# Kernel tuning notes

Measured on AMD Instinct MI355X. Metric: run time of the kernel, lower is better.

Reference implementation:

```python
import jax, jax.numpy as jnp
import numpy as np

ALPHA = 3.0


def _conv3x3(x, W, b):
    # x: [N, C, H, W]; W: [O, I, 3, 3]; SAME padding, stride 1 (matches Conv2d(dim, dim, 3, 1, 1))
    y = jax.lax.conv_general_dilated(
        x, W, window_strides=(1, 1), padding='SAME',
        dimension_numbers=('NCHW', 'OIHW', 'NCHW'))
    return y + b[None, :, None, None]


def setup_inputs() -> dict:
    key = jax.random.key(0)
    k = jax.random.split(key, 5)
    b, m, z, x, y = 2, 5, 64, 128, 256
    fan_in = z * 3 * 3
    bound = 1.0 / np.sqrt(fan_in)
    pts = jax.random.normal(k[0], (b, m, z, x, y), dtype=jnp.float32)
    W1 = jax.random.uniform(k[1], (z, z, 3, 3), jnp.float32, -bound, bound)
    b1 = jax.random.uniform(k[2], (z,), jnp.float32, -bound, bound)
    W2 = jax.random.uniform(k[3], (z, z, 3, 3), jnp.float32, -bound, bound)
    b2 = jax.random.uniform(k[4], (z,), jnp.float32, -bound, bound)
    return {"pts": pts, "W1": W1, "b1": b1, "W2": W2, "b2": b2}


def reference(pts, W1, b1, W2, b2):
    b, m, z, x, y = pts.shape
    flat = pts.reshape(b * m, z, x, y)
    n1 = jnp.tanh(ALPHA * _conv3x3(flat, W1, b1)).reshape(b, m, z, x, y)
    n2 = jnp.tanh(ALPHA * _conv3x3(flat, W2, b2)).reshape(b, m, z, x, y)
    # s[b,m,n,x,y] = sum_l n1[b,m,l,x,y] * n2[b,n,l,x,y]; second einsum is s with m,n swapped
    s = jnp.einsum('bmlxy,bnlxy->bmnxy', n1, n2)
    a = s - jnp.swapaxes(s, 1, 2)
    adj = jax.nn.sigmoid(ALPHA * a)
    adj = adj + jnp.eye(m, dtype=adj.dtype)[None, :, :, None, None]
    adj = adj / jnp.sum(adj, axis=2, keepdims=True)
    return adj
```

## Files before the change

kernel.cpp:

```cpp
#include <hip/hip_runtime.h>
#include <hip/hip_bf16.h>

typedef _Float16 f16x8 __attribute__((ext_vector_type(8)));
typedef _Float16 f16x4 __attribute__((ext_vector_type(4)));
typedef float f32x4 __attribute__((ext_vector_type(4)));
typedef unsigned short u16x8 __attribute__((ext_vector_type(8)));
typedef unsigned short u16x4 __attribute__((ext_vector_type(4)));

constexpr int B_ = 2, M_ = 5, C_ = 64, H_ = 128, W_ = 256;
constexpr int HW_ = H_ * W_;
constexpr int PLANE_ = C_ * HW_;
constexpr int NIMG_ = B_ * M_;
constexpr int PH_ = H_ + 2, PW_ = W_ + 2;

constexpr size_t OFF_XIN = 256;
constexpr size_t SZ_XIN  = (size_t)NIMG_ * PH_ * PW_ * 64 * 2;
constexpr size_t OFF_WL1 = OFF_XIN + SZ_XIN;
constexpr size_t SZ_WL   = (size_t)9 * 64 * 64 * 2;
constexpr size_t OFF_WL2 = OFF_WL1 + SZ_WL;
constexpr size_t OFF_N1  = OFF_WL2 + SZ_WL;
constexpr size_t SZ_N    = (size_t)NIMG_ * HW_ * 64 * 2;
constexpr size_t OFF_N2  = OFF_N1 + SZ_N;

__device__ inline bool sniff(const void* pts) {
  int lane = threadIdx.x & 63;
  unsigned short v = ((const unsigned short*)pts)[2 * lane];
  int e = (v >> 7) & 0xFF;
  unsigned long long mask = __ballot(e >= 100 && e <= 140);
  return __popcll(mask) >= 48;
}

__global__ __launch_bounds__(256) void prep_kernel(const void* __restrict__ in,
                                                   _Float16* __restrict__ xin,
                                                   const void* __restrict__ W1,
                                                   const void* __restrict__ W2,
                                                   _Float16* __restrict__ wl1,
                                                   _Float16* __restrict__ wl2) {
  __shared__ float sT[64 * 72];
  const int t = threadIdx.x;
  const bool isb = sniff(in);

  if (blockIdx.z == 10) {
    int s = blockIdx.y * 4 + blockIdx.x;
    if (s < 288) {
      int which = s / 144, blk = s - which * 144;
      int idx = blk * 256 + t;
      const void* Wsrc = which ? W2 : W1;
      _Float16* dst = which ? wl2 : wl1;
      int tap = idx >> 12;
      int oc = (idx >> 6) & 63;
      int ic = idx & 63;
      size_t so = (size_t)(oc * 64 + ic) * 9 + tap;
      float v = isb ? __bfloat162float(((const __hip_bfloat16*)Wsrc)[so])
                    : ((const float*)Wsrc)[so];
      dst[(tap * 4096 + oc * 64 + ic) ^ ((oc & 7) << 3)] = (_Float16)v;
    } else if (s < 320) {
      int idx = (s - 288) * 256 + t;
      if (idx >= NIMG_ * 772) return;
      int img = idx / 772, r = idx - img * 772;
      int ph, pw;
      if (r < 258)      { ph = 0;            pw = r; }
      else if (r < 516) { ph = PH_ - 1;      pw = r - 258; }
      else if (r < 644) { ph = r - 516 + 1;  pw = 0; }
      else              { ph = r - 644 + 1;  pw = PW_ - 1; }
      f16x8 z = {};
      _Float16* p = xin + ((size_t)(img * PH_ + ph) * PW_ + pw) * 64;
#pragma unroll
      for (int c8 = 0; c8 < 8; ++c8) *(f16x8*)(p + c8 * 8) = z;
    }
    return;
  }

  const int wt = blockIdx.x, h = blockIdx.y, img = blockIdx.z;
  const size_t ibase = (size_t)img * PLANE_ + (size_t)h * W_ + wt * 64;
  if (isb) {
#pragma unroll
    for (int k = 0; k < 2; ++k) {
      int u = k * 256 + t;
      int ic = u >> 3, wo = u & 7;
      const unsigned short* p = (const unsigned short*)in + ibase + (size_t)ic * HW_ + wo * 8;
      u16x8 v = *(const u16x8*)p;
#pragma unroll
      for (int j = 0; j < 8; ++j)
        sT[ic * 72 + wo * 8 + j] = __uint_as_float(((unsigned)v[j]) << 16);
    }
  } else {
#pragma unroll
    for (int k = 0; k < 4; ++k) {
      int u = k * 256 + t;
      int ic = u >> 4, wq = u & 15;
      const float* p = (const float*)in + ibase + (size_t)ic * HW_ + wq * 4;
      f32x4 v = *(const f32x4*)p;
      *(f32x4*)&sT[ic * 72 + wq * 4] = v;
    }
  }
  __syncthreads();
#pragma unroll
  for (int k = 0; k < 2; ++k) {
    int idx = k * 256 + t;
    int w = idx >> 3, c8 = idx & 7;
    f16x8 vv;
#pragma unroll
    for (int j = 0; j < 8; ++j) vv[j] = (_Float16)sT[(c8 * 8 + j) * 72 + w];
    int pw = wt * 64 + w + 1;
    size_t rowbase = ((size_t)(img * PH_ + (h + 1)) * PW_ + pw) * 128;
    int off = (c8 * 16) ^ ((pw & 7) << 4);
    *(f16x8*)((char*)xin + rowbase + off) = vv;
  }
}

__global__ __launch_bounds__(512, 2)
void conv_fused(const _Float16* __restrict__ xin,
                const _Float16* __restrict__ wl1, const _Float16* __restrict__ wl2,
                const void* __restrict__ bias1, const void* __restrict__ bias2,
                const void* __restrict__ pts,
                _Float16* __restrict__ n1, _Float16* __restrict__ n2) {
  __shared__ _Float16 sIn[10 * 66 * 64];
  __shared__ _Float16 sW[2 * 9 * 32 * 64];

  const int t = threadIdx.x;
  const int och = blockIdx.x & 1;
  const int pid = blockIdx.x >> 1;

  const int l = t & 63, wv = t >> 6;
  const int lr = l & 15, hi = l >> 4;
  const bool isb = sniff(pts);

#pragma unroll
  for (int c = 0; c < 2; ++c) {
    const f16x8* src = (const f16x8*)((const char*)(c ? wl2 : wl1) + och * 4096);
    f16x8* dst = (f16x8*)sW + c * 2304;
    for (int i = t; i < 2304; i += 512) {
      int tap = i >> 8, e = i & 255;
      dst[i] = src[tap * 512 + e];
    }
  }

  f32x4 bv1[2], bv2[2];
#pragma unroll
  for (int ob = 0; ob < 2; ++ob) {
    int oc0 = och * 32 + ob * 16 + hi * 4;
    if (isb) {
      u16x4 q1 = *(const u16x4*)((const unsigned short*)bias1 + oc0);
      u16x4 q2 = *(const u16x4*)((const unsigned short*)bias2 + oc0);
#pragma unroll
      for (int r = 0; r < 4; ++r) {
        bv1[ob][r] = __uint_as_float(((unsigned)q1[r]) << 16);
        bv2[ob][r] = __uint_as_float(((unsigned)q2[r]) << 16);
      }
    } else {
      bv1[ob] = *(const f32x4*)((const float*)bias1 + oc0);
      bv2[ob] = *(const f32x4*)((const float*)bias2 + oc0);
    }
  }

  int c2a[3][2], c2b[2];
#pragma unroll
  for (int dx = 0; dx < 3; ++dx) {
    int key = (((l & 7) + dx) & 7) << 4;
#pragma unroll
    for (int kw = 0; kw < 2; ++kw) c2a[dx][kw] = (hi * 16 + kw * 64) ^ key;
  }
#pragma unroll
  for (int kw = 0; kw < 2; ++kw) c2b[kw] = (hi * 16 + kw * 64) ^ ((l & 7) << 4);

  f16x8 rg[11];
  auto issue = [&](int tt) {
    int img = tt >> 6, hy = (tt >> 2) & 15, wx = tt & 3;
    const f16x8* base = (const f16x8*)(xin + ((size_t)(img * PH_ + hy * 8) * PW_ + wx * 64) * 64);
#pragma unroll
    for (int u = 0; u < 11; ++u) {
      int i = u * 512 + t;
      if (u < 10 || i < 5280) {
        int r = i / 528, cc = i - r * 528;
        rg[u] = base[(size_t)r * (PW_ * 8) + cc];
      }
    }
  };

  issue(pid);

  const char* sInB = (const char*)sIn;
  const char* sWB = (const char*)sW;

  __syncthreads();

#pragma unroll 1
  for (int j = 0; j < 5; ++j) {
    const int tt = pid + 128 * j;

#pragma unroll
    for (int u = 0; u < 11; ++u) {
      int i = u * 512 + t;
      if (u < 10 || i < 5280) ((f16x8*)sIn)[i] = rg[u];
    }
    asm volatile("s_waitcnt lgkmcnt(0)" ::: "memory");
    __builtin_amdgcn_s_barrier();

    if (j < 4) issue(pid + 128 * (j + 1));

    f32x4 acc1[4][2], acc2[4][2];
#pragma unroll
    for (int pa = 0; pa < 4; ++pa)
#pragma unroll
      for (int ob = 0; ob < 2; ++ob) {
        acc1[pa][ob] = bv1[ob];
        acc2[pa][ob] = bv2[ob];
      }

    __builtin_amdgcn_s_setprio(1);
#pragma unroll
    for (int ky = 0; ky < 3; ++ky) {
#pragma unroll
      for (int kx = 0; kx < 3; ++kx) {
        const int tap = ky * 3 + kx;
#pragma unroll
        for (int kw = 0; kw < 2; ++kw) {
          f16x8 a[4], b1a, b1b, b2a, b2b;
#pragma unroll
          for (int pa = 0; pa < 4; ++pa)
            a[pa] = *(const f16x8*)(sInB + ((wv + ky) * 8448 + (pa * 16 + lr + kx) * 128 + c2a[kx][kw]));
          b1a = *(const f16x8*)(sWB + tap * 4096 + lr * 128 + c2b[kw]);
          b1b = *(const f16x8*)(sWB + tap * 4096 + (16 + lr) * 128 + c2b[kw]);
          b2a = *(const f16x8*)(sWB + 36864 + tap * 4096 + lr * 128 + c2b[kw]);
          b2b = *(const f16x8*)(sWB + 36864 + tap * 4096 + (16 + lr) * 128 + c2b[kw]);
#pragma unroll
          for (int pa = 0; pa < 4; ++pa) {
            acc1[pa][0] = __builtin_amdgcn_mfma_f32_16x16x32_f16(b1a, a[pa], acc1[pa][0], 0, 0, 0);
            acc1[pa][1] = __builtin_amdgcn_mfma_f32_16x16x32_f16(b1b, a[pa], acc1[pa][1], 0, 0, 0);
            acc2[pa][0] = __builtin_amdgcn_mfma_f32_16x16x32_f16(b2a, a[pa], acc2[pa][0], 0, 0, 0);
            acc2[pa][1] = __builtin_amdgcn_mfma_f32_16x16x32_f16(b2b, a[pa], acc2[pa][1], 0, 0, 0);
          }
        }
      }
    }
    __builtin_amdgcn_s_setprio(0);

    __builtin_amdgcn_s_barrier();

    {
      int img = tt >> 6, hy = (tt >> 2) & 15, wx = tt & 3;
      size_t pxbase = ((size_t)(img * H_ + hy * 8 + wv) * W_ + wx * 64 + lr) * 64
                      + och * 32 + hi * 4;
#pragma unroll
      for (int pa = 0; pa < 4; ++pa)
#pragma unroll
        for (int ob = 0; ob < 2; ++ob) {
          size_t o = pxbase + (size_t)pa * (16 * 64) + ob * 16;
          f16x4 p1, p2;
#pragma unroll
          for (int r = 0; r < 4; ++r) {
            float e1 = __builtin_exp2f(acc1[pa][ob][r] * 8.656170245f);
            p1[r] = (_Float16)fmaf(-2.f, __builtin_amdgcn_rcpf(1.f + e1), 1.f);
            float e2 = __builtin_exp2f(acc2[pa][ob][r] * 8.656170245f);
            p2[r] = (_Float16)fmaf(-2.f, __builtin_amdgcn_rcpf(1.f + e2), 1.f);
          }
          *(f16x4*)(n1 + o) = p1;
          *(f16x4*)(n2 + o) = p2;
        }
    }
  }
}

__global__ __launch_bounds__(256)
void pairwise_kernel(const _Float16* __restrict__ n1, const _Float16* __restrict__ n2,
                     void* __restrict__ out, const void* __restrict__ pts) {
  const bool isb = sniff(pts);
  int tid = blockIdx.x * 256 + threadIdx.x;
  int gp = tid >> 3;
  int j = tid & 7;
  int b = gp >> 15, px = gp & (HW_ - 1);
  const _Float16* p1 = n1 + ((size_t)(b * M_) * HW_ + px) * 64 + j * 8;
  const _Float16* p2 = n2 + ((size_t)(b * M_) * HW_ + px) * 64 + j * 8;

  f16x8 A[M_], Bv[M_];
#pragma unroll
  for (int m = 0; m < M_; ++m) {
    A[m]  = *(const f16x8*)(p1 + (size_t)m * PLANE_);
    Bv[m] = *(const f16x8*)(p2 + (size_t)m * PLANE_);
  }

  float s[M_][M_];
#pragma unroll
  for (int m = 0; m < M_; ++m)
#pragma unroll
    for (int n = 0; n < M_; ++n) s[m][n] = 0.f;

#pragma unroll
  for (int jj = 0; jj < 8; ++jj)
#pragma unroll
    for (int m = 0; m < M_; ++m)
#pragma unroll
      for (int n = 0; n < M_; ++n)
        s[m][n] += (float)A[m][jj] * (float)Bv[n][jj];

#pragma unroll
  for (int m = 0; m < M_; ++m)
#pragma unroll
    for (int n = 0; n < M_; ++n) {
      s[m][n] += __shfl_xor(s[m][n], 1);
      s[m][n] += __shfl_xor(s[m][n], 2);
      s[m][n] += __shfl_xor(s[m][n], 4);
    }

  float adj[M_][M_], rs[M_];
#pragma unroll
  for (int m = 0; m < M_; ++m) {
    float r = 0.f;
#pragma unroll
    for (int n = 0; n < M_; ++n) {
      float a = s[m][n] - s[n][m];
      float e = __builtin_exp2f(a * -4.328085123f);
      float v = __builtin_amdgcn_rcpf(1.f + e);
      if (m == n) v += 1.f;
      adj[m][n] = v;
      r += v;
    }
    rs[m] = r;
  }

  for (int k = j; k < 25; k += 8) {
    int m = k / 5, n = k - m * 5;
    float v = adj[m][n] * __builtin_amdgcn_rcpf(rs[m]);
    size_t o = ((size_t)((b * M_ + m) * M_ + n)) * HW_ + px;
    if (isb) ((__hip_bfloat16*)out)[o] = __float2bfloat16(v);
    else     ((float*)out)[o] = v;
  }
}

extern "C" void kernel_launch(void* const* d_in, const int* in_sizes, int n_in,
                              void* d_out, int out_size, void* d_ws, size_t ws_size,
                              hipStream_t stream) {
  const void* pts = d_in[0];
  const void* W1  = d_in[1];
  const void* b1  = d_in[2];
  const void* W2  = d_in[3];
  const void* b2  = d_in[4];

  char* ws = (char*)d_ws;
  _Float16* xin = (_Float16*)(ws + OFF_XIN);
  _Float16* wl1 = (_Float16*)(ws + OFF_WL1);
  _Float16* wl2 = (_Float16*)(ws + OFF_WL2);
  _Float16* n1  = (_Float16*)(ws + OFF_N1);
  _Float16* n2  = (_Float16*)(ws + OFF_N2);

  prep_kernel<<<dim3(4, H_, NIMG_ + 1), dim3(256), 0, stream>>>(pts, xin, W1, W2, wl1, wl2);
  conv_fused<<<dim3(256), dim3(512), 0, stream>>>(xin, wl1, wl2, b1, b2, pts, n1, n2);
  pairwise_kernel<<<dim3(B_ * HW_ * 8 / 256), dim3(256), 0, stream>>>(n1, n2, d_out, pts);
}
```

Measured before the change: 111.7 us.

## Fuse input transpose and padding into conv kernel, drop padded staging buffer

Removes the prep kernel that transposed NCHW input into a padded, swizzled fp16 NHWC workspace. The conv kernel now gathers directly from the original input, with per-element bounds checks for the halo and on-the-fly conversion to fp16, and writes each tile into shared memory using the swizzled layout. This saves a full write and re-read of the padded intermediate plus one kernel launch. The cost is strided scalar global loads (eight channel planes per vector) in place of contiguous 16-byte loads, which may coalesce poorly and add latency to the prefetch.

```diff
diff --git a/kernel.cpp b/kernel.cpp
--- a/kernel.cpp
+++ b/kernel.cpp
@@ -11,11 +11,8 @@
 constexpr int HW_ = H_ * W_;
 constexpr int PLANE_ = C_ * HW_;
 constexpr int NIMG_ = B_ * M_;
-constexpr int PH_ = H_ + 2, PW_ = W_ + 2;
-
-constexpr size_t OFF_XIN = 256;
-constexpr size_t SZ_XIN  = (size_t)NIMG_ * PH_ * PW_ * 64 * 2;
-constexpr size_t OFF_WL1 = OFF_XIN + SZ_XIN;
+
+constexpr size_t OFF_WL1 = 256;
 constexpr size_t SZ_WL   = (size_t)9 * 64 * 64 * 2;
 constexpr size_t OFF_WL2 = OFF_WL1 + SZ_WL;
 constexpr size_t OFF_N1  = OFF_WL2 + SZ_WL;
@@ -30,90 +27,26 @@
   return __popcll(mask) >= 48;
 }
 
-__global__ __launch_bounds__(256) void prep_kernel(const void* __restrict__ in,
-                                                   _Float16* __restrict__ xin,
-                                                   const void* __restrict__ W1,
-                                                   const void* __restrict__ W2,
-                                                   _Float16* __restrict__ wl1,
-                                                   _Float16* __restrict__ wl2) {
-  __shared__ float sT[64 * 72];
-  const int t = threadIdx.x;
-  const bool isb = sniff(in);
-
-  if (blockIdx.z == 10) {
-    int s = blockIdx.y * 4 + blockIdx.x;
-    if (s < 288) {
-      int which = s / 144, blk = s - which * 144;
-      int idx = blk * 256 + t;
-      const void* Wsrc = which ? W2 : W1;
-      _Float16* dst = which ? wl2 : wl1;
-      int tap = idx >> 12;
-      int oc = (idx >> 6) & 63;
-      int ic = idx & 63;
-      size_t so = (size_t)(oc * 64 + ic) * 9 + tap;
-      float v = isb ? __bfloat162float(((const __hip_bfloat16*)Wsrc)[so])
-                    : ((const float*)Wsrc)[so];
-      dst[(tap * 4096 + oc * 64 + ic) ^ ((oc & 7) << 3)] = (_Float16)v;
-    } else if (s < 320) {
-      int idx = (s - 288) * 256 + t;
-      if (idx >= NIMG_ * 772) return;
-      int img = idx / 772, r = idx - img * 772;
-      int ph, pw;
-      if (r < 258)      { ph = 0;            pw = r; }
-      else if (r < 516) { ph = PH_ - 1;      pw = r - 258; }
-      else if (r < 644) { ph = r - 516 + 1;  pw = 0; }
-      else              { ph = r - 644 + 1;  pw = PW_ - 1; }
-      f16x8 z = {};
-      _Float16* p = xin + ((size_t)(img * PH_ + ph) * PW_ + pw) * 64;
-#pragma unroll
-      for (int c8 = 0; c8 < 8; ++c8) *(f16x8*)(p + c8 * 8) = z;
-    }
-    return;
-  }
-
-  const int wt = blockIdx.x, h = blockIdx.y, img = blockIdx.z;
-  const size_t ibase = (size_t)img * PLANE_ + (size_t)h * W_ + wt * 64;
-  if (isb) {
-#pragma unroll
-    for (int k = 0; k < 2; ++k) {
-      int u = k * 256 + t;
-      int ic = u >> 3, wo = u & 7;
-      const unsigned short* p = (const unsigned short*)in + ibase + (size_t)ic * HW_ + wo * 8;
-      u16x8 v = *(const u16x8*)p;
-#pragma unroll
-      for (int j = 0; j < 8; ++j)
-        sT[ic * 72 + wo * 8 + j] = __uint_as_float(((unsigned)v[j]) << 16);
-    }
-  } else {
-#pragma unroll
-    for (int k = 0; k < 4; ++k) {
-      int u = k * 256 + t;
-      int ic = u >> 4, wq = u & 15;
-      const float* p = (const float*)in + ibase + (size_t)ic * HW_ + wq * 4;
-      f32x4 v = *(const f32x4*)p;
-      *(f32x4*)&sT[ic * 72 + wq * 4] = v;
-    }
-  }
-  __syncthreads();
-#pragma unroll
-  for (int k = 0; k < 2; ++k) {
-    int idx = k * 256 + t;
-    int w = idx >> 3, c8 = idx & 7;
-    f16x8 vv;
-#pragma unroll
-    for (int j = 0; j < 8; ++j) vv[j] = (_Float16)sT[(c8 * 8 + j) * 72 + w];
-    int pw = wt * 64 + w + 1;
-    size_t rowbase = ((size_t)(img * PH_ + (h + 1)) * PW_ + pw) * 128;
-    int off = (c8 * 16) ^ ((pw & 7) << 4);
-    *(f16x8*)((char*)xin + rowbase + off) = vv;
-  }
+__global__ void wprep_kernel(const void* __restrict__ W1, const void* __restrict__ W2,
+                             _Float16* __restrict__ wl1, _Float16* __restrict__ wl2,
+                             const void* __restrict__ pts) {
+  const bool isb = sniff(pts);
+  int idx = blockIdx.x * 256 + threadIdx.x;
+  const void* Wsrc = blockIdx.y ? W2 : W1;
+  _Float16* dst = blockIdx.y ? wl2 : wl1;
+  int tap = idx >> 12;
+  int oc = (idx >> 6) & 63;
+  int ic = idx & 63;
+  size_t s = (size_t)(oc * 64 + ic) * 9 + tap;
+  float v = isb ? __bfloat162float(((const __hip_bfloat16*)Wsrc)[s])
+                : ((const float*)Wsrc)[s];
+  dst[(tap * 4096 + oc * 64 + ic) ^ ((oc & 7) << 3)] = (_Float16)v;
 }
 
 __global__ __launch_bounds__(512, 2)
-void conv_fused(const _Float16* __restrict__ xin,
+void conv_fused(const void* __restrict__ pts,
                 const _Float16* __restrict__ wl1, const _Float16* __restrict__ wl2,
                 const void* __restrict__ bias1, const void* __restrict__ bias2,
-                const void* __restrict__ pts,
                 _Float16* __restrict__ n1, _Float16* __restrict__ n2) {
   __shared__ _Float16 sIn[10 * 66 * 64];
   __shared__ _Float16 sW[2 * 9 * 32 * 64];
@@ -164,17 +97,46 @@
 #pragma unroll
   for (int kw = 0; kw < 2; ++kw) c2b[kw] = (hi * 16 + kw * 64) ^ ((l & 7) << 4);
 
+  int rr[11], ppu[11], lof[11], gof[11];
+#pragma unroll
+  for (int u = 0; u < 11; ++u) {
+    int i = u * 512 + t;
+    if (i >= 5280) i = 5279;
+    int c8 = i / 660, rem = i - c8 * 660;
+    int r = rem / 66, p = rem - r * 66;
+    rr[u] = r;
+    ppu[u] = p;
+    lof[u] = r * 8448 + p * 128 + ((c8 * 16) ^ ((p & 7) << 4));
+    gof[u] = c8 * 8 * HW_ + r * W_ + p;
+  }
+
   f16x8 rg[11];
   auto issue = [&](int tt) {
     int img = tt >> 6, hy = (tt >> 2) & 15, wx = tt & 3;
-    const f16x8* base = (const f16x8*)(xin + ((size_t)(img * PH_ + hy * 8) * PW_ + wx * 64) * 64);
+    int h0 = hy * 8 - 1, p0 = wx * 64 - 1;
+    int tbase = img * PLANE_ + h0 * W_ + p0;
 #pragma unroll
     for (int u = 0; u < 11; ++u) {
-      int i = u * 512 + t;
-      if (u < 10 || i < 5280) {
-        int r = i / 528, cc = i - r * 528;
-        rg[u] = base[(size_t)r * (PW_ * 8) + cc];
+      if (u == 10 && (5120 + t) >= 5280) continue;
+      int hin = h0 + rr[u];
+      int pin = p0 + ppu[u];
+      bool ok = ((unsigned)hin < (unsigned)H_) && ((unsigned)pin < (unsigned)W_);
+      int g = tbase + gof[u];
+      f16x8 v = {};
+      if (ok) {
+        if (isb) {
+          const unsigned short* sp = (const unsigned short*)pts + g;
+#pragma unroll
+          for (int jj = 0; jj < 8; ++jj)
+            v[jj] = (_Float16)__uint_as_float(((unsigned)sp[(size_t)jj * HW_]) << 16);
+        } else {
+          const float* sp = (const float*)pts + g;
+#pragma unroll
+          for (int jj = 0; jj < 8; ++jj)
+            v[jj] = (_Float16)sp[(size_t)jj * HW_];
+        }
       }
+      rg[u] = v;
     }
   };
 
@@ -191,8 +153,8 @@
 
 #pragma unroll
     for (int u = 0; u < 11; ++u) {
-      int i = u * 512 + t;
-      if (u < 10 || i < 5280) ((f16x8*)sIn)[i] = rg[u];
+      if (u == 10 && (5120 + t) >= 5280) continue;
+      *(f16x8*)((char*)sIn + lof[u]) = rg[u];
     }
     asm volatile("s_waitcnt lgkmcnt(0)" ::: "memory");
     __builtin_amdgcn_s_barrier();
@@ -338,13 +300,12 @@
   const void* b2  = d_in[4];
 
   char* ws = (char*)d_ws;
-  _Float16* xin = (_Float16*)(ws + OFF_XIN);
   _Float16* wl1 = (_Float16*)(ws + OFF_WL1);
   _Float16* wl2 = (_Float16*)(ws + OFF_WL2);
   _Float16* n1  = (_Float16*)(ws + OFF_N1);
   _Float16* n2  = (_Float16*)(ws + OFF_N2);
 
-  prep_kernel<<<dim3(4, H_, NIMG_ + 1), dim3(256), 0, stream>>>(pts, xin, W1, W2, wl1, wl2);
-  conv_fused<<<dim3(256), dim3(512), 0, stream>>>(xin, wl1, wl2, b1, b2, pts, n1, n2);
+  wprep_kernel<<<dim3(144, 2), dim3(256), 0, stream>>>(W1, W2, wl1, wl2, pts);
+  conv_fused<<<dim3(256), dim3(512), 0, stream>>>(pts, wl1, wl2, b1, b2, n1, n2);
   pairwise_kernel<<<dim3(B_ * HW_ * 8 / 256), dim3(256), 0, stream>>>(n1, n2, d_out, pts);
 }
```

After: 133.0 us. +19.1%, slower.

## Overlap tanh epilogue of previous tile with MFMA loop of current tile

Applied to the files above, without the earlier changes.

Double-buffers the conv accumulators and fully unrolls the five-tile loop so that the tanh and store epilogue of tile j-1 is interleaved, one chunk per tap, into the MFMA loop of tile j. The last tile's epilogue runs after the loop. This is meant to hide the transcendental math and global stores behind matrix-core work. It doubles the accumulator register footprint, which could lower occupancy or cause spills, and it makes the code larger.

```diff
diff --git a/kernel.cpp b/kernel.cpp
--- a/kernel.cpp
+++ b/kernel.cpp
@@ -185,8 +185,31 @@
 
   __syncthreads();
 
-#pragma unroll 1
-  for (int j = 0; j < 5; ++j) {
+  f32x4 aA1[4][2], aA2[4][2], aB1[4][2], aB2[4][2];
+
+  auto pxbase_of = [&](int tt) -> size_t {
+    int img = tt >> 6, hy = (tt >> 2) & 15, wx = tt & 3;
+    return ((size_t)(img * H_ + hy * 8 + wv) * W_ + wx * 64 + lr) * 64
+           + och * 32 + hi * 4;
+  };
+
+  auto epi_chunk = [&](f32x4 (&p1a)[4][2], f32x4 (&p2a)[4][2], size_t pxbase,
+                       int pa, int ob) {
+    size_t o = pxbase + (size_t)pa * (16 * 64) + ob * 16;
+    f16x4 p1, p2;
+#pragma unroll
+    for (int r = 0; r < 4; ++r) {
+      float e1 = __builtin_exp2f(p1a[pa][ob][r] * 8.656170245f);
+      p1[r] = (_Float16)fmaf(-2.f, __builtin_amdgcn_rcpf(1.f + e1), 1.f);
+      float e2 = __builtin_exp2f(p2a[pa][ob][r] * 8.656170245f);
+      p2[r] = (_Float16)fmaf(-2.f, __builtin_amdgcn_rcpf(1.f + e2), 1.f);
+    }
+    *(f16x4*)(n1 + o) = p1;
+    *(f16x4*)(n2 + o) = p2;
+  };
+
+  auto body = [&](int j, f32x4 (&cur1)[4][2], f32x4 (&cur2)[4][2],
+                  f32x4 (&prv1)[4][2], f32x4 (&prv2)[4][2], bool hasPrev) {
     const int tt = pid + 128 * j;
 
 #pragma unroll
@@ -197,15 +220,16 @@
     asm volatile("s_waitcnt lgkmcnt(0)" ::: "memory");
     __builtin_amdgcn_s_barrier();
 
-    if (j < 4) issue(pid + 128 * (j + 1));
-
-    f32x4 acc1[4][2], acc2[4][2];
+    if (j < 4) issue(tt + 128);
+
+    size_t ppx = hasPrev ? pxbase_of(tt - 128) : 0;
+
 #pragma unroll
     for (int pa = 0; pa < 4; ++pa)
 #pragma unroll
       for (int ob = 0; ob < 2; ++ob) {
-        acc1[pa][ob] = bv1[ob];
-        acc2[pa][ob] = bv2[ob];
+        cur1[pa][ob] = bv1[ob];
+        cur2[pa][ob] = bv2[ob];
       }
 
     __builtin_amdgcn_s_setprio(1);
@@ -226,39 +250,32 @@
           b2b = *(const f16x8*)(sWB + 36864 + tap * 4096 + (16 + lr) * 128 + c2b[kw]);
 #pragma unroll
           for (int pa = 0; pa < 4; ++pa) {
-            acc1[pa][0] = __builtin_amdgcn_mfma_f32_16x16x32_f16(b1a, a[pa], acc1[pa][0], 0, 0, 0);
-            acc1[pa][1] = __builtin_amdgcn_mfma_f32_16x16x32_f16(b1b, a[pa], acc1[pa][1], 0, 0, 0);
-            acc2[pa][0] = __builtin_amdgcn_mfma_f32_16x16x32_f16(b2a, a[pa], acc2[pa][0], 0, 0, 0);
-            acc2[pa][1] = __builtin_amdgcn_mfma_f32_16x16x32_f16(b2b, a[pa], acc2[pa][1], 0, 0, 0);
+            cur1[pa][0] = __builtin_amdgcn_mfma_f32_16x16x32_f16(b1a, a[pa], cur1[pa][0], 0, 0, 0);
+            cur1[pa][1] = __builtin_amdgcn_mfma_f32_16x16x32_f16(b1b, a[pa], cur1[pa][1], 0, 0, 0);
+            cur2[pa][0] = __builtin_amdgcn_mfma_f32_16x16x32_f16(b2a, a[pa], cur2[pa][0], 0, 0, 0);
+            cur2[pa][1] = __builtin_amdgcn_mfma_f32_16x16x32_f16(b2b, a[pa], cur2[pa][1], 0, 0, 0);
           }
         }
+        if (hasPrev && tap < 8) epi_chunk(prv1, prv2, ppx, tap >> 1, tap & 1);
       }
     }
     __builtin_amdgcn_s_setprio(0);
 
     __builtin_amdgcn_s_barrier();
-
-    {
-      int img = tt >> 6, hy = (tt >> 2) & 15, wx = tt & 3;
-      size_t pxbase = ((size_t)(img * H_ + hy * 8 + wv) * W_ + wx * 64 + lr) * 64
-                      + och * 32 + hi * 4;
-#pragma unroll
-      for (int pa = 0; pa < 4; ++pa)
-#pragma unroll
-        for (int ob = 0; ob < 2; ++ob) {
-          size_t o = pxbase + (size_t)pa * (16 * 64) + ob * 16;
-          f16x4 p1, p2;
-#pragma unroll
-          for (int r = 0; r < 4; ++r) {
-            float e1 = __builtin_exp2f(acc1[pa][ob][r] * 8.656170245f);
-            p1[r] = (_Float16)fmaf(-2.f, __builtin_amdgcn_rcpf(1.f + e1), 1.f);
-            float e2 = __builtin_exp2f(acc2[pa][ob][r] * 8.656170245f);
-            p2[r] = (_Float16)fmaf(-2.f, __builtin_amdgcn_rcpf(1.f + e2), 1.f);
-          }
-          *(f16x4*)(n1 + o) = p1;
-          *(f16x4*)(n2 + o) = p2;
-        }
-    }
+  };
+
+  body(0, aA1, aA2, aB1, aB2, false);
+  body(1, aB1, aB2, aA1, aA2, true);
+  body(2, aA1, aA2, aB1, aB2, true);
+  body(3, aB1, aB2, aA1, aA2, true);
+  body(4, aA1, aA2, aB1, aB2, true);
+
+  {
+    size_t ppx = pxbase_of(pid + 512);
+#pragma unroll
+    for (int pa = 0; pa < 4; ++pa)
+#pragma unroll
+      for (int ob = 0; ob < 2; ++ob) epi_chunk(aA1, aA2, ppx, pa, ob);
   }
 }
 
```

Result: slower. 117.2 us (+4.9%).
